# Optimization experiments

Hardware: AMD Instinct MI355X
Metric: run time of the kernel (lower is better)

## Reference

```python
import jax, jax.numpy as jnp
import numpy as np

HEADS = 4
DIM_HEAD = 128
SCALE = DIM_HEAD ** (-0.5)


def setup_inputs() -> dict:
    key = jax.random.key(0)
    k1, k2 = jax.random.split(key)
    fmap = jax.random.normal(k1, (1, 256, 64, 64), dtype=jnp.float32)
    # 1x1 conv weight, no bias: [out_channels=2*heads*dim_head, in_channels=dim]
    W_qk = jax.random.normal(k2, (1024, 256), dtype=jnp.float32) * (256 ** -0.5)
    return {"fmap": fmap, "W_qk": W_qk}


def reference(fmap, W_qk):
    b, c, h, w = fmap.shape
    # 1x1 conv == channel-wise matmul
    qk = jnp.einsum('bcxy,oc->boxy', fmap, W_qk)  # [b, 2*heads*dim_head, h, w]
    q, k = jnp.split(qk, 2, axis=1)
    def to_bhxyd(t):
        # 'b (h d) x y -> b h x y d'
        return t.reshape(b, HEADS, DIM_HEAD, h, w).transpose(0, 1, 3, 4, 2)
    q = to_bhxyd(q) * SCALE
    k = to_bhxyd(k)
    sim = jnp.einsum('bhxyd,bhuvd->bhxyuv', q, k)
    sim = sim.reshape(b, HEADS, h * w, h * w)
    return jax.nn.softmax(sim, axis=-1)
```

## Files before the change

kernel.cpp:

```cpp
#include <hip/hip_runtime.h>
#include <math.h>

#define HEADS 4
#define DHEAD 128
#define NPOS  4096
#define CIN   256
#define SCALEF 0.08838834764831845f
#define LOG2E  1.4426950408889634f
#define QSCALE (SCALEF * LOG2E)

typedef _Float16 half8  __attribute__((ext_vector_type(8)));
typedef _Float16 half4  __attribute__((ext_vector_type(4)));
typedef _Float16 half2v __attribute__((ext_vector_type(2)));
typedef float    f32x4  __attribute__((ext_vector_type(4)));

#define FRAG_HEAD_HALVES (256 * 4 * 512)

__global__ __launch_bounds__(256) void cvt_kernel(const float* __restrict__ fmap,
                                                  const float* __restrict__ W,
                                                  _Float16* __restrict__ W16,
                                                  _Float16* __restrict__ fmapT) {
  if (blockIdx.x < 16) {
    int base = blockIdx.x * 16384 + threadIdx.x;
#pragma unroll
    for (int t = 0; t < 64; ++t) {
      int idx = base + t * 256;
      float v = W[idx];
      W16[idx] = (_Float16)(idx < 512 * CIN ? v * QSCALE : v);
    }
  } else {
    int tile = blockIdx.x - 16;
    int p0 = (tile >> 2) * 64, c0 = (tile & 3) * 64;
    __shared__ float t_lds[64][65];
    int tid = threadIdx.x;
#pragma unroll
    for (int t = 0; t < 16; ++t) {
      int lin = tid + t * 256;
      int r = lin >> 6, col = lin & 63;
      t_lds[r][col] = fmap[(size_t)(c0 + r) * NPOS + p0 + col];
    }
    __syncthreads();
#pragma unroll
    for (int t = 0; t < 16; ++t) {
      int lin = tid + t * 256;
      int pr = lin >> 6, cc = lin & 63;
      fmapT[(size_t)(p0 + pr) * CIN + c0 + cc] = (_Float16)t_lds[cc][pr];
    }
  }
}

__global__ __launch_bounds__(256) void proj_mfma(const _Float16* __restrict__ W16,
                                                 const _Float16* __restrict__ fmapT,
                                                 _Float16* __restrict__ qf,
                                                 _Float16* __restrict__ kf) {
  const int p0 = blockIdx.x * 64;
  const int o0 = blockIdx.y * 64 + (threadIdx.x >> 6) * 16;
  const int l = threadIdx.x & 63;
  const int lr = l & 15, lg = l >> 4;

  const f32x4 z = {0.f, 0.f, 0.f, 0.f};
  f32x4 acc[4] = {z, z, z, z};
#pragma unroll
  for (int kb = 0; kb < 8; ++kb) {
    half8 a = *(const half8*)(W16 + (size_t)(o0 + lr) * CIN + kb * 32 + lg * 8);
#pragma unroll
    for (int j = 0; j < 4; ++j) {
      half8 b = *(const half8*)(fmapT + (size_t)(p0 + j * 16 + lr) * CIN + kb * 32 + lg * 8);
      acc[j] = __builtin_amdgcn_mfma_f32_16x16x32_f16(a, b, acc[j], 0, 0, 0);
    }
  }
  const int ob = o0 + lg * 4;
  const bool isq = ob < 512;
  const int oo = isq ? ob : ob - 512;
  const int h = oo >> 7, db = oo & 127;
  const int kb2 = db >> 5;
  const int flane = ((db >> 3) & 3) * 16 + lr;
  const int e0 = db & 7;
  _Float16* dst = (isq ? qf : kf) + (size_t)h * FRAG_HEAD_HALVES;
#pragma unroll
  for (int j = 0; j < 4; ++j) {
    int pt = (p0 >> 4) + j;
    half4 v = {(_Float16)acc[j][0], (_Float16)acc[j][1],
               (_Float16)acc[j][2], (_Float16)acc[j][3]};
    *(half4*)(dst + ((size_t)pt * 4 + kb2) * 512 + flane * 8 + e0) = v;
  }
}

#define QROWS 16
#define NTIL  32

__global__ __launch_bounds__(512) void attn_mfma(const _Float16* __restrict__ qf,
                                                 const _Float16* __restrict__ kf,
                                                 float* __restrict__ out) {
  const int b = blockIdx.x;
  const int h = (b & 7) >> 1;
  const int qtile = ((b >> 3) << 1) | (b & 1);
  const int i0 = qtile * QROWS;

  const int wv = threadIdx.x >> 6;
  const int l = threadIdx.x & 63;
  const int lr = l & 15, lg = l >> 4;

  const _Float16* Qf = qf + (size_t)h * FRAG_HEAD_HALVES;
  const _Float16* Kf = kf + (size_t)h * FRAG_HEAD_HALVES;

  half8 afr[4];
#pragma unroll
  for (int kb = 0; kb < 4; ++kb)
    afr[kb] = *(const half8*)(Qf + ((size_t)(i0 >> 4) * 4 + kb) * 512 + l * 8);

  const int jt0 = wv * NTIL;
  half2v Pst[2 * NTIL];
  float rs[4] = {0.f, 0.f, 0.f, 0.f};
  const f32x4 z = {0.f, 0.f, 0.f, 0.f};

#pragma unroll
  for (int t = 0; t < NTIL; ++t) {
    const _Float16* kp = Kf + ((size_t)(jt0 + t) * 4) * 512 + l * 8;
    half8 b0 = *(const half8*)(kp);
    half8 b1 = *(const half8*)(kp + 512);
    half8 b2 = *(const half8*)(kp + 1024);
    half8 b3 = *(const half8*)(kp + 1536);
    f32x4 acc = z;
    __builtin_amdgcn_s_setprio(1);
    acc = __builtin_amdgcn_mfma_f32_16x16x32_f16(afr[0], b0, acc, 0, 0, 0);
    acc = __builtin_amdgcn_mfma_f32_16x16x32_f16(afr[1], b1, acc, 0, 0, 0);
    acc = __builtin_amdgcn_mfma_f32_16x16x32_f16(afr[2], b2, acc, 0, 0, 0);
    acc = __builtin_amdgcn_mfma_f32_16x16x32_f16(afr[3], b3, acc, 0, 0, 0);
    __builtin_amdgcn_s_setprio(0);
    float e0 = __builtin_amdgcn_exp2f(acc[0]);
    float e1 = __builtin_amdgcn_exp2f(acc[1]);
    float e2 = __builtin_amdgcn_exp2f(acc[2]);
    float e3 = __builtin_amdgcn_exp2f(acc[3]);
    rs[0] += e0; rs[1] += e1; rs[2] += e2; rs[3] += e3;
    Pst[2 * t]     = half2v{(_Float16)e0, (_Float16)e1};
    Pst[2 * t + 1] = half2v{(_Float16)e2, (_Float16)e3};
  }

#pragma unroll
  for (int off = 1; off < 16; off <<= 1) {
#pragma unroll
    for (int r = 0; r < 4; ++r) rs[r] += __shfl_xor(rs[r], off);
  }
  __shared__ float red[8][16];
  if (lr == 0) {
#pragma unroll
    for (int r = 0; r < 4; ++r) red[wv][lg * 4 + r] = rs[r];
  }
  __syncthreads();
  float inv[4];
#pragma unroll
  for (int r = 0; r < 4; ++r) {
    float s = 0.f;
#pragma unroll
    for (int w = 0; w < 8; ++w) s += red[w][lg * 4 + r];
    inv[r] = 1.0f / s;
  }

  float* ob = out + ((size_t)h * NPOS + i0) * NPOS + jt0 * 16;
#pragma unroll
  for (int t = 0; t < NTIL; ++t) {
    float e[4] = {(float)Pst[2 * t][0], (float)Pst[2 * t][1],
                  (float)Pst[2 * t + 1][0], (float)Pst[2 * t + 1][1]};
#pragma unroll
    for (int r = 0; r < 4; ++r) {
      ob[(size_t)(lg * 4 + r) * NPOS + t * 16 + lr] = e[r] * inv[r];
    }
  }
}

extern "C" void kernel_launch(void* const* d_in, const int* in_sizes, int n_in,
                              void* d_out, int out_size, void* d_ws, size_t ws_size,
                              hipStream_t stream) {
  const float* fmap = (const float*)d_in[0];
  const float* W    = (const float*)d_in[1];
  float* out = (float*)d_out;

  char* ws = (char*)d_ws;
  _Float16* qf    = (_Float16*)(ws);
  _Float16* kf    = (_Float16*)(ws + (4u << 20));
  _Float16* W16   = (_Float16*)(ws + (8u << 20));
  _Float16* fmapT = (_Float16*)(ws + (8u << 20) + (512u << 10));

  cvt_kernel<<<272, 256, 0, stream>>>(fmap, W, W16, fmapT);
  proj_mfma<<<dim3(NPOS / 64, 1024 / 64), 256, 0, stream>>>(W16, fmapT, qf, kf);
  attn_mfma<<<NPOS / QROWS * HEADS, 512, 0, stream>>>(qf, kf, out);
}
```

Measured before the change: 107.0 us.

## Stage softmax output through swizzled LDS for coalesced 16-byte global stores

Each wave now takes interleaved key tiles (tile t*8+wave) rather than a contiguous range. The normalized probabilities are written into a 64KB swizzled LDS buffer in four column chunks, then read back and stored to global memory as 16-byte vectors covering contiguous row segments. The old path issued scattered 4-byte stores with a 16-float stride pattern. The row-sum reduction is also computed once by 16 threads and broadcast. This adds four rounds of LDS traffic and barriers, and the large LDS allocation may reduce occupancy.

```diff
diff --git a/kernel.cpp b/kernel.cpp
--- a/kernel.cpp
+++ b/kernel.cpp
@@ -101,6 +101,10 @@
   const int l = threadIdx.x & 63;
   const int lr = l & 15, lg = l >> 4;
 
+  __shared__ __align__(16) float lds_buf[16 * 1024];
+  __shared__ float red[8][16];
+  __shared__ float rowinv[16];
+
   const _Float16* Qf = qf + (size_t)h * FRAG_HEAD_HALVES;
   const _Float16* Kf = kf + (size_t)h * FRAG_HEAD_HALVES;
 
@@ -109,14 +113,15 @@
   for (int kb = 0; kb < 4; ++kb)
     afr[kb] = *(const half8*)(Qf + ((size_t)(i0 >> 4) * 4 + kb) * 512 + l * 8);
 
-  const int jt0 = wv * NTIL;
+  const _Float16* kbase = Kf + (size_t)wv * 2048 + l * 8;
+
   half2v Pst[2 * NTIL];
   float rs[4] = {0.f, 0.f, 0.f, 0.f};
   const f32x4 z = {0.f, 0.f, 0.f, 0.f};
 
 #pragma unroll
   for (int t = 0; t < NTIL; ++t) {
-    const _Float16* kp = Kf + ((size_t)(jt0 + t) * 4) * 512 + l * 8;
+    const _Float16* kp = kbase + (size_t)t * 16384;
     half8 b0 = *(const half8*)(kp);
     half8 b1 = *(const half8*)(kp + 512);
     half8 b2 = *(const half8*)(kp + 1024);
@@ -142,30 +147,52 @@
 #pragma unroll
     for (int r = 0; r < 4; ++r) rs[r] += __shfl_xor(rs[r], off);
   }
-  __shared__ float red[8][16];
   if (lr == 0) {
 #pragma unroll
     for (int r = 0; r < 4; ++r) red[wv][lg * 4 + r] = rs[r];
+  }
+  __syncthreads();
+  if (threadIdx.x < 16) {
+    float s = 0.f;
+#pragma unroll
+    for (int w = 0; w < 8; ++w) s += red[w][threadIdx.x];
+    rowinv[threadIdx.x] = 1.0f / s;
   }
   __syncthreads();
   float inv[4];
 #pragma unroll
-  for (int r = 0; r < 4; ++r) {
-    float s = 0.f;
-#pragma unroll
-    for (int w = 0; w < 8; ++w) s += red[w][lg * 4 + r];
-    inv[r] = 1.0f / s;
-  }
-
-  float* ob = out + ((size_t)h * NPOS + i0) * NPOS + jt0 * 16;
-#pragma unroll
-  for (int t = 0; t < NTIL; ++t) {
-    float e[4] = {(float)Pst[2 * t][0], (float)Pst[2 * t][1],
-                  (float)Pst[2 * t + 1][0], (float)Pst[2 * t + 1][1]};
-#pragma unroll
-    for (int r = 0; r < 4; ++r) {
-      ob[(size_t)(lg * 4 + r) * NPOS + t * 16 + lr] = e[r] * inv[r];
-    }
+  for (int r = 0; r < 4; ++r) inv[r] = rowinv[lg * 4 + r];
+
+  float* obase = out + ((size_t)h * NPOS + i0) * NPOS;
+  const int swz = lg << 3;
+
+#pragma unroll
+  for (int c = 0; c < 4; ++c) {
+#pragma unroll
+    for (int j = 0; j < 8; ++j) {
+      int k = c * 8 + j;
+      int colw = (8 * j + wv) * 16 + lr;
+      float e0 = (float)Pst[2 * k][0] * inv[0];
+      float e1 = (float)Pst[2 * k][1] * inv[1];
+      float e2 = (float)Pst[2 * k + 1][0] * inv[2];
+      float e3 = (float)Pst[2 * k + 1][1] * inv[3];
+      int dwb = (lg * 4) * 1024 + colw;
+      lds_buf[(dwb)          ^ swz] = e0;
+      lds_buf[(dwb + 1024)   ^ swz] = e1;
+      lds_buf[(dwb + 2048)   ^ swz] = e2;
+      lds_buf[(dwb + 3072)   ^ swz] = e3;
+    }
+    __syncthreads();
+#pragma unroll
+    for (int s = 0; s < 8; ++s) {
+      int ig = wv * 8 + s;
+      int row = ig >> 2;
+      int q = ig & 3;
+      int dw = (row * 1024 + q * 256 + l * 4) ^ ((row >> 2) << 3);
+      f32x4 v = *(const f32x4*)&lds_buf[dw];
+      *(f32x4*)&obase[(size_t)row * NPOS + c * 1024 + q * 256 + l * 4] = v;
+    }
+    __syncthreads();
   }
 }
 
```

Result: slower. 116.5 us (+8.9%).

## Double-buffer K fragments via global_load_lds DMA in attention kernel

Applied to the files above, without the earlier changes.

Replaces direct global-to-register loads of K fragments with asynchronous global_load_lds transfers into a per-wave double-buffered LDS stage, using manual vmcnt waits. The aim is to overlap the fetch of the next K tile with the MFMA and exp work on the current one, hiding global load latency. It adds 64KB of LDS per block, which may reduce occupancy. Correctness depends on the hand-placed waitcnts and the LDS write layout of the DMA builtin; there is no wave barrier, which is fine only because each buffer is private to its wave.

```diff
diff --git a/kernel.cpp b/kernel.cpp
--- a/kernel.cpp
+++ b/kernel.cpp
@@ -101,6 +101,9 @@
   const int l = threadIdx.x & 63;
   const int lr = l & 15, lg = l >> 4;
 
+  __shared__ __align__(16) _Float16 kstage[2][8][2048];
+  __shared__ float red[8][16];
+
   const _Float16* Qf = qf + (size_t)h * FRAG_HEAD_HALVES;
   const _Float16* Kf = kf + (size_t)h * FRAG_HEAD_HALVES;
 
@@ -110,39 +113,70 @@
     afr[kb] = *(const half8*)(Qf + ((size_t)(i0 >> 4) * 4 + kb) * 512 + l * 8);
 
   const int jt0 = wv * NTIL;
+  const _Float16* kbase = Kf + (size_t)jt0 * 2048 + l * 8;
+
   half2v Pst[2 * NTIL];
   float rs[4] = {0.f, 0.f, 0.f, 0.f};
   const f32x4 z = {0.f, 0.f, 0.f, 0.f};
 
-#pragma unroll
-  for (int t = 0; t < NTIL; ++t) {
-    const _Float16* kp = Kf + ((size_t)(jt0 + t) * 4) * 512 + l * 8;
-    half8 b0 = *(const half8*)(kp);
-    half8 b1 = *(const half8*)(kp + 512);
-    half8 b2 = *(const half8*)(kp + 1024);
-    half8 b3 = *(const half8*)(kp + 1536);
-    f32x4 acc = z;
-    __builtin_amdgcn_s_setprio(1);
-    acc = __builtin_amdgcn_mfma_f32_16x16x32_f16(afr[0], b0, acc, 0, 0, 0);
-    acc = __builtin_amdgcn_mfma_f32_16x16x32_f16(afr[1], b1, acc, 0, 0, 0);
-    acc = __builtin_amdgcn_mfma_f32_16x16x32_f16(afr[2], b2, acc, 0, 0, 0);
-    acc = __builtin_amdgcn_mfma_f32_16x16x32_f16(afr[3], b3, acc, 0, 0, 0);
-    __builtin_amdgcn_s_setprio(0);
-    float e0 = __builtin_amdgcn_exp2f(acc[0]);
-    float e1 = __builtin_amdgcn_exp2f(acc[1]);
-    float e2 = __builtin_amdgcn_exp2f(acc[2]);
-    float e3 = __builtin_amdgcn_exp2f(acc[3]);
-    rs[0] += e0; rs[1] += e1; rs[2] += e2; rs[3] += e3;
-    Pst[2 * t]     = half2v{(_Float16)e0, (_Float16)e1};
-    Pst[2 * t + 1] = half2v{(_Float16)e2, (_Float16)e3};
-  }
+#define DMA(buf, tt)                                                          \
+  { const _Float16* kp_ = kbase + (size_t)(tt) * 2048;                        \
+    __builtin_amdgcn_global_load_lds(                                         \
+        (const __attribute__((address_space(1))) unsigned int*)(kp_),         \
+        (__attribute__((address_space(3))) unsigned int*)(&kstage[buf][wv][0]), 16, 0, 0);  \
+    __builtin_amdgcn_global_load_lds(                                         \
+        (const __attribute__((address_space(1))) unsigned int*)(kp_ + 512),   \
+        (__attribute__((address_space(3))) unsigned int*)(&kstage[buf][wv][512]), 16, 0, 0); \
+    __builtin_amdgcn_global_load_lds(                                         \
+        (const __attribute__((address_space(1))) unsigned int*)(kp_ + 1024),  \
+        (__attribute__((address_space(3))) unsigned int*)(&kstage[buf][wv][1024]), 16, 0, 0); \
+    __builtin_amdgcn_global_load_lds(                                         \
+        (const __attribute__((address_space(1))) unsigned int*)(kp_ + 1536),  \
+        (__attribute__((address_space(3))) unsigned int*)(&kstage[buf][wv][1536]), 16, 0, 0); }
+
+#define COMPUTE(buf, tt)                                                      \
+  { const _Float16* sp = &kstage[buf][wv][l * 8];                             \
+    half8 b0 = *(const half8*)(sp);                                           \
+    half8 b1 = *(const half8*)(sp + 512);                                     \
+    half8 b2 = *(const half8*)(sp + 1024);                                    \
+    half8 b3 = *(const half8*)(sp + 1536);                                    \
+    f32x4 acc = z;                                                            \
+    __builtin_amdgcn_s_setprio(1);                                            \
+    acc = __builtin_amdgcn_mfma_f32_16x16x32_f16(afr[0], b0, acc, 0, 0, 0);   \
+    acc = __builtin_amdgcn_mfma_f32_16x16x32_f16(afr[1], b1, acc, 0, 0, 0);   \
+    acc = __builtin_amdgcn_mfma_f32_16x16x32_f16(afr[2], b2, acc, 0, 0, 0);   \
+    acc = __builtin_amdgcn_mfma_f32_16x16x32_f16(afr[3], b3, acc, 0, 0, 0);   \
+    __builtin_amdgcn_s_setprio(0);                                            \
+    float e0 = __builtin_amdgcn_exp2f(acc[0]);                                \
+    float e1 = __builtin_amdgcn_exp2f(acc[1]);                                \
+    float e2 = __builtin_amdgcn_exp2f(acc[2]);                                \
+    float e3 = __builtin_amdgcn_exp2f(acc[3]);                                \
+    rs[0] += e0; rs[1] += e1; rs[2] += e2; rs[3] += e3;                       \
+    Pst[2 * (tt)]     = half2v{(_Float16)e0, (_Float16)e1};                   \
+    Pst[2 * (tt) + 1] = half2v{(_Float16)e2, (_Float16)e3}; }
+
+  DMA(0, 0)
+#pragma unroll
+  for (int tp = 0; tp < NTIL; tp += 2) {
+    DMA(1, tp + 1)
+    asm volatile("s_waitcnt vmcnt(4)" ::: "memory");
+    COMPUTE(0, tp)
+    if (tp + 2 < NTIL) {
+      DMA(0, tp + 2)
+      asm volatile("s_waitcnt vmcnt(4)" ::: "memory");
+    } else {
+      asm volatile("s_waitcnt vmcnt(0)" ::: "memory");
+    }
+    COMPUTE(1, tp + 1)
+  }
+#undef DMA
+#undef COMPUTE
 
 #pragma unroll
   for (int off = 1; off < 16; off <<= 1) {
 #pragma unroll
     for (int r = 0; r < 4; ++r) rs[r] += __shfl_xor(rs[r], off);
   }
-  __shared__ float red[8][16];
   if (lr == 0) {
 #pragma unroll
     for (int r = 0; r < 4; ++r) red[wv][lg * 4 + r] = rs[r];
```

Result: no change. 105.5 us, median of 2 (-1.4%).

## Process two query tiles per attention block, overlapping tile B compute with tile A stores

Applied to the files above, without the earlier changes.

Each attention block now handles two consecutive 16-row query tiles. It computes the exponentials for tile B while writing out the normalized results of tile A, so MFMA/exp work overlaps the large output store stream. The grid shrinks to 512 blocks. In exchange, register pressure roughly doubles from holding two P buffers, which may cut occupancy or cause spills, and fewer blocks reduces parallelism across CUs.

```diff
diff --git a/kernel.cpp b/kernel.cpp
--- a/kernel.cpp
+++ b/kernel.cpp
@@ -94,79 +94,125 @@
                                                  float* __restrict__ out) {
   const int b = blockIdx.x;
   const int h = (b & 7) >> 1;
-  const int qtile = ((b >> 3) << 1) | (b & 1);
-  const int i0 = qtile * QROWS;
+  const int pairidx = ((b >> 3) << 1) | (b & 1);
+  const int qtA = pairidx * 2;
+  const int qtB = qtA + 1;
 
   const int wv = threadIdx.x >> 6;
   const int l = threadIdx.x & 63;
   const int lr = l & 15, lg = l >> 4;
 
+  __shared__ float red[8][16];
+
   const _Float16* Qf = qf + (size_t)h * FRAG_HEAD_HALVES;
   const _Float16* Kf = kf + (size_t)h * FRAG_HEAD_HALVES;
 
+  const int jt0 = wv * NTIL;
+  const _Float16* kbase = Kf + (size_t)jt0 * 2048 + l * 8;
+
+  const f32x4 z = {0.f, 0.f, 0.f, 0.f};
+
+#define COMPUTE_TILE(PDST, RS, AFR, tt)                                       \
+  { const _Float16* kp = kbase + (size_t)(tt) * 2048;                         \
+    half8 b0 = *(const half8*)(kp);                                           \
+    half8 b1 = *(const half8*)(kp + 512);                                     \
+    half8 b2 = *(const half8*)(kp + 1024);                                    \
+    half8 b3 = *(const half8*)(kp + 1536);                                    \
+    f32x4 acc = z;                                                            \
+    __builtin_amdgcn_s_setprio(1);                                            \
+    acc = __builtin_amdgcn_mfma_f32_16x16x32_f16(AFR[0], b0, acc, 0, 0, 0);   \
+    acc = __builtin_amdgcn_mfma_f32_16x16x32_f16(AFR[1], b1, acc, 0, 0, 0);   \
+    acc = __builtin_amdgcn_mfma_f32_16x16x32_f16(AFR[2], b2, acc, 0, 0, 0);   \
+    acc = __builtin_amdgcn_mfma_f32_16x16x32_f16(AFR[3], b3, acc, 0, 0, 0);   \
+    __builtin_amdgcn_s_setprio(0);                                            \
+    float e0 = __builtin_amdgcn_exp2f(acc[0]);                                \
+    float e1 = __builtin_amdgcn_exp2f(acc[1]);                                \
+    float e2 = __builtin_amdgcn_exp2f(acc[2]);                                \
+    float e3 = __builtin_amdgcn_exp2f(acc[3]);                                \
+    RS[0] += e0; RS[1] += e1; RS[2] += e2; RS[3] += e3;                       \
+    PDST[2 * (tt)]     = half2v{(_Float16)e0, (_Float16)e1};                  \
+    PDST[2 * (tt) + 1] = half2v{(_Float16)e2, (_Float16)e3}; }
+
   half8 afr[4];
 #pragma unroll
   for (int kb = 0; kb < 4; ++kb)
-    afr[kb] = *(const half8*)(Qf + ((size_t)(i0 >> 4) * 4 + kb) * 512 + l * 8);
-
-  const int jt0 = wv * NTIL;
-  half2v Pst[2 * NTIL];
-  float rs[4] = {0.f, 0.f, 0.f, 0.f};
-  const f32x4 z = {0.f, 0.f, 0.f, 0.f};
-
-#pragma unroll
-  for (int t = 0; t < NTIL; ++t) {
-    const _Float16* kp = Kf + ((size_t)(jt0 + t) * 4) * 512 + l * 8;
-    half8 b0 = *(const half8*)(kp);
-    half8 b1 = *(const half8*)(kp + 512);
-    half8 b2 = *(const half8*)(kp + 1024);
-    half8 b3 = *(const half8*)(kp + 1536);
-    f32x4 acc = z;
-    __builtin_amdgcn_s_setprio(1);
-    acc = __builtin_amdgcn_mfma_f32_16x16x32_f16(afr[0], b0, acc, 0, 0, 0);
-    acc = __builtin_amdgcn_mfma_f32_16x16x32_f16(afr[1], b1, acc, 0, 0, 0);
-    acc = __builtin_amdgcn_mfma_f32_16x16x32_f16(afr[2], b2, acc, 0, 0, 0);
-    acc = __builtin_amdgcn_mfma_f32_16x16x32_f16(afr[3], b3, acc, 0, 0, 0);
-    __builtin_amdgcn_s_setprio(0);
-    float e0 = __builtin_amdgcn_exp2f(acc[0]);
-    float e1 = __builtin_amdgcn_exp2f(acc[1]);
-    float e2 = __builtin_amdgcn_exp2f(acc[2]);
-    float e3 = __builtin_amdgcn_exp2f(acc[3]);
-    rs[0] += e0; rs[1] += e1; rs[2] += e2; rs[3] += e3;
-    Pst[2 * t]     = half2v{(_Float16)e0, (_Float16)e1};
-    Pst[2 * t + 1] = half2v{(_Float16)e2, (_Float16)e3};
-  }
+    afr[kb] = *(const half8*)(Qf + ((size_t)qtA * 4 + kb) * 512 + l * 8);
+
+  half2v PA[2 * NTIL];
+  float rsA[4] = {0.f, 0.f, 0.f, 0.f};
+#pragma unroll
+  for (int t = 0; t < NTIL; ++t) COMPUTE_TILE(PA, rsA, afr, t)
 
 #pragma unroll
   for (int off = 1; off < 16; off <<= 1) {
 #pragma unroll
-    for (int r = 0; r < 4; ++r) rs[r] += __shfl_xor(rs[r], off);
-  }
-  __shared__ float red[8][16];
+    for (int r = 0; r < 4; ++r) rsA[r] += __shfl_xor(rsA[r], off);
+  }
   if (lr == 0) {
 #pragma unroll
-    for (int r = 0; r < 4; ++r) red[wv][lg * 4 + r] = rs[r];
+    for (int r = 0; r < 4; ++r) red[wv][lg * 4 + r] = rsA[r];
   }
   __syncthreads();
-  float inv[4];
+  float invA[4];
 #pragma unroll
   for (int r = 0; r < 4; ++r) {
     float s = 0.f;
 #pragma unroll
     for (int w = 0; w < 8; ++w) s += red[w][lg * 4 + r];
-    inv[r] = 1.0f / s;
-  }
-
-  float* ob = out + ((size_t)h * NPOS + i0) * NPOS + jt0 * 16;
+    invA[r] = 1.0f / s;
+  }
+
+  half8 afrB[4];
+#pragma unroll
+  for (int kb = 0; kb < 4; ++kb)
+    afrB[kb] = *(const half8*)(Qf + ((size_t)qtB * 4 + kb) * 512 + l * 8);
+
+  float* obA = out + ((size_t)h * NPOS + qtA * QROWS) * NPOS + jt0 * 16;
+  float* obB = out + ((size_t)h * NPOS + qtB * QROWS) * NPOS + jt0 * 16;
+
+  half2v PB[2 * NTIL];
+  float rsB[4] = {0.f, 0.f, 0.f, 0.f};
 #pragma unroll
   for (int t = 0; t < NTIL; ++t) {
-    float e[4] = {(float)Pst[2 * t][0], (float)Pst[2 * t][1],
-                  (float)Pst[2 * t + 1][0], (float)Pst[2 * t + 1][1]};
+    COMPUTE_TILE(PB, rsB, afrB, t)
+    float eA[4] = {(float)PA[2 * t][0], (float)PA[2 * t][1],
+                   (float)PA[2 * t + 1][0], (float)PA[2 * t + 1][1]};
 #pragma unroll
     for (int r = 0; r < 4; ++r) {
-      ob[(size_t)(lg * 4 + r) * NPOS + t * 16 + lr] = e[r] * inv[r];
-    }
-  }
+      obA[(size_t)(lg * 4 + r) * NPOS + t * 16 + lr] = eA[r] * invA[r];
+    }
+  }
+
+  __syncthreads();
+#pragma unroll
+  for (int off = 1; off < 16; off <<= 1) {
+#pragma unroll
+    for (int r = 0; r < 4; ++r) rsB[r] += __shfl_xor(rsB[r], off);
+  }
+  if (lr == 0) {
+#pragma unroll
+    for (int r = 0; r < 4; ++r) red[wv][lg * 4 + r] = rsB[r];
+  }
+  __syncthreads();
+  float invB[4];
+#pragma unroll
+  for (int r = 0; r < 4; ++r) {
+    float s = 0.f;
+#pragma unroll
+    for (int w = 0; w < 8; ++w) s += red[w][lg * 4 + r];
+    invB[r] = 1.0f / s;
+  }
+
+#pragma unroll
+  for (int t = 0; t < NTIL; ++t) {
+    float eB[4] = {(float)PB[2 * t][0], (float)PB[2 * t][1],
+                   (float)PB[2 * t + 1][0], (float)PB[2 * t + 1][1]};
+#pragma unroll
+    for (int r = 0; r < 4; ++r) {
+      obB[(size_t)(lg * 4 + r) * NPOS + t * 16 + lr] = eB[r] * invB[r];
+    }
+  }
+#undef COMPUTE_TILE
 }
 
 extern "C" void kernel_launch(void* const* d_in, const int* in_sizes, int n_in,
@@ -184,5 +230,5 @@
 
   cvt_kernel<<<272, 256, 0, stream>>>(fmap, W, W16, fmapT);
   proj_mfma<<<dim3(NPOS / 64, 1024 / 64), 256, 0, stream>>>(W16, fmapT, qf, kf);
-  attn_mfma<<<NPOS / QROWS * HEADS, 512, 0, stream>>>(qf, kf, out);
-}
+  attn_mfma<<<512, 512, 0, stream>>>(qf, kf, out);
+}
```

After: 319.7 us. 199% more time.
